# Performance work log

Measured on AMD Instinct MI355X. Metric: run time of the kernel, lower is better.

The kernel has to match this reference:

```python
import jax, jax.numpy as jnp
import numpy as np

B = 2048        # batch
C = 64          # args.embed_size (channel dim; attention runs over this axis)
N = 11          # spatial rows per window
D = 11          # args.hsi_windowSize
SA = N * D      # args.size_SA = 121, Linear in/out size
HID = 128       # args.hid_router
NUM_PATH = 4    # num_out_path


def setup_inputs() -> dict:
    key = jax.random.key(0)
    ks = jax.random.split(key, 12)
    w = lambda k, shape: (jax.random.normal(k, shape, dtype=jnp.float32) * 0.05)
    return {
        "lidar": jax.random.normal(ks[0], (B, C, N, D), dtype=jnp.float32),
        "hsi": jax.random.normal(ks[1], (B, C, N, D), dtype=jnp.float32),
        # Cross_Self_attention linears (shared module, used in both directions)
        "Wq": w(ks[2], (SA, SA)), "bq": jnp.zeros((SA,), jnp.float32),
        "Wk": w(ks[3], (SA, SA)), "bk": jnp.zeros((SA,), jnp.float32),
        "Wv": w(ks[4], (SA, SA)), "bv": jnp.zeros((SA,), jnp.float32),
        # Router MLP: Linear(2C, HID) -> ReLU -> Linear(HID, NUM_PATH) -> softmax
        "Wr1": w(ks[5], (2 * C, HID)), "br1": jnp.zeros((HID,), jnp.float32),
        "Wr2": w(ks[6], (HID, NUM_PATH)), "br2": jnp.zeros((NUM_PATH,), jnp.float32),
        # 1x1 Conv2d(2C -> C): pure channel mixing
        "Wc": w(ks[7], (C, 2 * C)), "bc": jnp.zeros((C,), jnp.float32),
    }


def reference(lidar, hsi, Wq, bq, Wk, bk, Wv, bv, Wr1, br1, Wr2, br2, Wc, bc):
    def cross_sa(x, y):
        # x, y: [B, C, SA]; Linear acts on last dim (size_SA)
        q = x @ Wq.T + bq                                   # [B, C, SA]
        k = x @ Wk.T + bk                                   # [B, C, SA]
        v = y @ Wv.T + bv                                   # [B, C, SA]
        scores = jnp.einsum('bhs,bgs->bhg', q, k)           # [B, C, C] attn over channels
        probs = jax.nn.softmax(scores, axis=-1)
        # custom: attn @ (Q * V) elementwise gate instead of attn @ V
        return jnp.einsum('bhg,bgs->bhs', probs, q * v)     # [B, C, SA]
        # dropout(0.5) is identity in eval mode

    # router on channel-concat of raw inputs
    pooled = jnp.concatenate([lidar, hsi], axis=1).mean(axis=(2, 3))   # [B, 2C]
    path_prob = jax.nn.softmax(jax.nn.relu(pooled @ Wr1 + br1) @ Wr2 + br2, axis=-1)

    l = lidar.reshape(B, C, SA)
    h = hsi.reshape(B, C, SA)
    h_emb = cross_sa(l, h).reshape(B, C, N, D)
    l_emb = cross_sa(h, l).reshape(B, C, N, D)

    cat = jnp.concatenate([l_emb, h_emb], axis=1)                       # [B, 2C, N, D]
    emb = jnp.einsum('oc,bchw->bohw', Wc, cat) + bc[None, :, None, None]
    return (emb, path_prob)
```

## Files before the change

### kernel.cpp

```cpp
#include <hip/hip_runtime.h>
#include <hip/hip_bf16.h>

#define NB 2048
#define SA 121
#define EMB_TOTAL (NB * 64 * SA)

typedef short bf16x8 __attribute__((ext_vector_type(8)));
typedef float f32x4  __attribute__((ext_vector_type(4)));
typedef unsigned int u32x2 __attribute__((ext_vector_type(2)));

__device__ __forceinline__ short f2bf(float f) {
    union { __hip_bfloat16 h; short s; } u;
    u.h = __float2bfloat16(f);
    return u.s;
}
__device__ __forceinline__ unsigned pack2(float a, float b) {
    union { __hip_bfloat16 h[2]; unsigned u; } p;
    p.h[0] = __float2bfloat16(a);
    p.h[1] = __float2bfloat16(b);
    return p.u;
}

#define MFMA(a, b, c) __builtin_amdgcn_mfma_f32_16x16x32_bf16((a), (b), (c), 0, 0, 0)

__global__ void convert_weights(const float* __restrict__ Wq, const float* __restrict__ Wk,
                                const float* __restrict__ Wv, const float* __restrict__ Wc,
                                const float* __restrict__ bq, short* __restrict__ ws) {
    int i = blockIdx.x * 256 + threadIdx.x;
    if (i < 16384) {
        int t = i >> 7, s = i & 127;
        float acc = 0.f;
        if (t < SA && s < SA)
            for (int j = 0; j < SA; ++j) acc += Wq[j * SA + s] * Wk[j * SA + t];
        ws[i] = f2bf(acc);
    } else if (i < 32768) {
        int j = i - 16384; int r = j >> 7, c = j & 127;
        ws[i] = f2bf((r < SA && c < SA) ? Wq[r * SA + c] : 0.f);
    } else if (i < 49152) {
        int j = i - 32768; int r = j >> 7, c = j & 127;
        ws[i] = f2bf((r < SA && c < SA) ? Wv[r * SA + c] : 0.f);
    } else if (i < 57344) {
        ws[i] = f2bf(Wc[i - 49152]);
    } else if (i < 57472) {
        int t = i - 57344;
        float acc = 0.f;
        if (t < SA)
            for (int j = 0; j < SA; ++j) acc += bq[j] * Wk[j * SA + t];
        ((float*)(ws + 57344))[t] = acc;
    }
}

__launch_bounds__(256, 2)
__global__ void fused_kernel(const float* __restrict__ lidar, const float* __restrict__ hsi,
                             const float* __restrict__ bq, const float* __restrict__ bv,
                             const float* __restrict__ Wr1, const float* __restrict__ br1,
                             const float* __restrict__ Wr2, const float* __restrict__ br2,
                             const float* __restrict__ bc,
                             const short* __restrict__ wsb, float* __restrict__ out) {
    __shared__ __align__(16) short sA[64 * 136];
    __shared__ __align__(16) short sB[64 * 136];
    __shared__ __align__(16) short sD[64 * 136];
    __shared__ __align__(16) short sG[128 * 72];
    __shared__ __align__(16) short sE[64 * 72];
    __shared__ float sR[388];

    const int tid  = threadIdx.x;
    const int b    = blockIdx.x;
    const int lane = tid & 63;
    const int wid  = tid >> 6;
    const int l16  = lane & 15;
    const int g16  = lane >> 4;

    const short* WA = wsb;
    const short* WQ = wsb + 16384;
    const short* WV = wsb + 32768;
    const short* WC = wsb + 49152;
    const float* wvp = (const float*)(wsb + 57344);

    bf16x8 wwa[2][4], wqf[2][4], wvf[2][4];
    #pragma unroll
    for (int nn = 0; nn < 2; ++nn) {
        const int rw = ((wid * 2 + nn) * 16 + l16) * 128 + g16 * 8;
        #pragma unroll
        for (int k0 = 0; k0 < 4; ++k0) {
            wwa[nn][k0] = *(const bf16x8*)&WA[rw + k0 * 32];
            wqf[nn][k0] = *(const bf16x8*)&WQ[rw + k0 * 32];
            wvf[nn][k0] = *(const bf16x8*)&WV[rw + k0 * 32];
        }
    }
    bf16x8 wcf[2][2];
    {
        const int rw = (wid * 16 + l16) * 128 + g16 * 8;
        #pragma unroll
        for (int cb = 0; cb < 2; ++cb)
            #pragma unroll
            for (int k0 = 0; k0 < 2; ++k0)
                wcf[cb][k0] = *(const bf16x8*)&WC[rw + cb * 64 + k0 * 32];
    }
    float bqv[2], bvv2[2];
    #pragma unroll
    for (int nn = 0; nn < 2; ++nn) {
        int sc_ = (wid * 2 + nn) * 16 + l16;
        bool ok = sc_ < SA;
        bqv[nn]  = ok ? bq[sc_] : 0.f;
        bvv2[nn] = ok ? bv[sc_] : 0.f;
    }

    {
        const int row = wid * 16 + l16;
        const float* gA = lidar + (size_t)b * 7744 + row * 121;
        const float* gB = hsi   + (size_t)b * 7744 + row * 121;
        float rsA = 0.f, rsB = 0.f, wA = 0.f, wB = 0.f;
        #pragma unroll
        for (int k0 = 0; k0 < 4; ++k0) {
            const int c0 = k0 * 32 + g16 * 8;
            bf16x8 a, h;
            if (c0 == 120) {
                float xa = gA[120], xb = gB[120], wv0 = wvp[120];
                rsA += xa; rsB += xb; wA += xa * wv0; wB += xb * wv0;
                a[0] = f2bf(xa); h[0] = f2bf(xb);
                #pragma unroll
                for (int j = 1; j < 8; ++j) { a[j] = 0; h[j] = 0; }
            } else {
                #pragma unroll
                for (int j = 0; j < 8; ++j) {
                    float xa = gA[c0 + j], xb = gB[c0 + j];
                    float wv0 = wvp[c0 + j];
                    rsA += xa; rsB += xb;
                    wA += xa * wv0; wB += xb * wv0;
                    a[j] = f2bf(xa); h[j] = f2bf(xb);
                }
            }
            *(bf16x8*)&sA[row * 136 + c0] = a;
            *(bf16x8*)&sB[row * 136 + c0] = h;
        }
        rsA += __shfl_xor(rsA, 16, 64); rsA += __shfl_xor(rsA, 32, 64);
        rsB += __shfl_xor(rsB, 16, 64); rsB += __shfl_xor(rsB, 32, 64);
        wA  += __shfl_xor(wA, 16, 64);  wA  += __shfl_xor(wA, 32, 64);
        wB  += __shfl_xor(wB, 16, 64);  wB  += __shfl_xor(wB, 32, 64);
        if (g16 == 0) {
            sR[row] = rsA * (1.f / 121.f);
            sR[64 + row] = rsB * (1.f / 121.f);
            sR[128 + row] = wA;
            sR[192 + row] = wB;
        }
    }
    __syncthreads();

    f32x4 eacc[8];
    #pragma unroll
    for (int n = 0; n < 8; ++n) eacc[n] = (f32x4){0.f, 0.f, 0.f, 0.f};

    #pragma unroll 1
    for (int dir = 0; dir < 2; ++dir) {
        const short* Xqk = dir ? sB : sA;
        const short* Xv  = dir ? sA : sB;
        const int cb = dir ? 0 : 1;

        #pragma unroll
        for (int m = 0; m < 4; ++m) {
            bf16x8 afr[4], vfr[4];
            #pragma unroll
            for (int k0 = 0; k0 < 4; ++k0) {
                afr[k0] = *(const bf16x8*)&Xqk[(m * 16 + l16) * 136 + k0 * 32 + g16 * 8];
                vfr[k0] = *(const bf16x8*)&Xv [(m * 16 + l16) * 136 + k0 * 32 + g16 * 8];
            }
            f32x4 ya[2], qa[2], va[2];
            ya[0] = (f32x4){0,0,0,0}; ya[1] = (f32x4){0,0,0,0};
            qa[0] = (f32x4){0,0,0,0}; qa[1] = (f32x4){0,0,0,0};
            va[0] = (f32x4){0,0,0,0}; va[1] = (f32x4){0,0,0,0};
            #pragma unroll
            for (int k0 = 0; k0 < 4; ++k0) {
                ya[0] = MFMA(afr[k0], wwa[0][k0], ya[0]);
                ya[1] = MFMA(afr[k0], wwa[1][k0], ya[1]);
                qa[0] = MFMA(afr[k0], wqf[0][k0], qa[0]);
                qa[1] = MFMA(afr[k0], wqf[1][k0], qa[1]);
                va[0] = MFMA(vfr[k0], wvf[0][k0], va[0]);
                va[1] = MFMA(vfr[k0], wvf[1][k0], va[1]);
            }
            #pragma unroll
            for (int nn = 0; nn < 2; ++nn) {
                const int sc_ = (wid * 2 + nn) * 16 + l16;
                #pragma unroll
                for (int r = 0; r < 4; ++r)
                    sD[(m * 16 + g16 * 4 + r) * 136 + sc_] = f2bf(ya[nn][r]);
                float g0 = (va[nn][0] + bvv2[nn]) * (qa[nn][0] + bqv[nn]);
                float g1 = (va[nn][1] + bvv2[nn]) * (qa[nn][1] + bqv[nn]);
                float g2 = (va[nn][2] + bvv2[nn]) * (qa[nn][2] + bqv[nn]);
                float g3 = (va[nn][3] + bvv2[nn]) * (qa[nn][3] + bqv[nn]);
                u32x2 pk;
                pk.x = pack2(g0, g1);
                pk.y = pack2(g2, g3);
                *(u32x2*)&sG[sc_ * 72 + m * 16 + g16 * 4] = pk;
            }
        }
        __syncthreads();

        {
            f32x4 sc4[4];
            #pragma unroll
            for (int n = 0; n < 4; ++n) sc4[n] = (f32x4){0,0,0,0};
            #pragma unroll
            for (int k0 = 0; k0 < 4; ++k0) {
                bf16x8 afr = *(const bf16x8*)&sD[(wid * 16 + l16) * 136 + k0 * 32 + g16 * 8];
                #pragma unroll
                for (int n = 0; n < 4; ++n) {
                    bf16x8 bfr = *(const bf16x8*)&Xqk[(n * 16 + l16) * 136 + k0 * 32 + g16 * 8];
                    sc4[n] = MFMA(afr, bfr, sc4[n]);
                }
            }
            float wg[4];
            #pragma unroll
            for (int n = 0; n < 4; ++n) wg[n] = sR[128 + dir * 64 + n * 16 + l16];
            float p[4][4];
            #pragma unroll
            for (int r = 0; r < 4; ++r) {
                float s0 = sc4[0][r] + wg[0], s1 = sc4[1][r] + wg[1];
                float s2 = sc4[2][r] + wg[2], s3 = sc4[3][r] + wg[3];
                float mx = fmaxf(fmaxf(s0, s1), fmaxf(s2, s3));
                #pragma unroll
                for (int off = 1; off < 16; off <<= 1) mx = fmaxf(mx, __shfl_xor(mx, off, 64));
                float e0 = exp2f((s0 - mx) * 1.44269504f);
                float e1 = exp2f((s1 - mx) * 1.44269504f);
                float e2 = exp2f((s2 - mx) * 1.44269504f);
                float e3 = exp2f((s3 - mx) * 1.44269504f);
                float sum = e0 + e1 + e2 + e3;
                #pragma unroll
                for (int off = 1; off < 16; off <<= 1) sum += __shfl_xor(sum, off, 64);
                float inv = 1.f / sum;
                p[0][r] = e0 * inv; p[1][r] = e1 * inv; p[2][r] = e2 * inv; p[3][r] = e3 * inv;
            }
            #pragma unroll
            for (int n = 0; n < 4; ++n) {
                u32x2 pk;
                pk.x = pack2(p[n][0], p[n][1]);
                pk.y = pack2(p[n][2], p[n][3]);
                *(u32x2*)&sE[(n * 16 + l16) * 72 + wid * 16 + g16 * 4] = pk;
            }
        }
        __syncthreads();

        {
            f32x4 macc[4];
            #pragma unroll
            for (int n = 0; n < 4; ++n) macc[n] = (f32x4){0,0,0,0};
            #pragma unroll
            for (int k0 = 0; k0 < 2; ++k0)
                #pragma unroll
                for (int n = 0; n < 4; ++n) {
                    bf16x8 bfr = *(const bf16x8*)&sE[(n * 16 + l16) * 72 + k0 * 32 + g16 * 8];
                    macc[n] = MFMA(wcf[cb][k0], bfr, macc[n]);
                }
            #pragma unroll
            for (int n = 0; n < 4; ++n)
                #pragma unroll
                for (int r = 0; r < 4; ++r)
                    sD[(wid * 16 + g16 * 4 + r) * 72 + n * 16 + l16] = f2bf(macc[n][r]);
        }
        __syncthreads();

        #pragma unroll
        for (int k0 = 0; k0 < 2; ++k0) {
            bf16x8 afr = *(const bf16x8*)&sD[(wid * 16 + l16) * 72 + k0 * 32 + g16 * 8];
            #pragma unroll
            for (int n = 0; n < 8; ++n) {
                bf16x8 bfr = *(const bf16x8*)&sG[(n * 16 + l16) * 72 + k0 * 32 + g16 * 8];
                eacc[n] = MFMA(afr, bfr, eacc[n]);
            }
        }
        __syncthreads();
    }

    float* eo = out + (size_t)b * 7744;
    {
        float bcv[4];
        #pragma unroll
        for (int r = 0; r < 4; ++r) bcv[r] = bc[wid * 16 + g16 * 4 + r];
        #pragma unroll
        for (int n = 0; n < 8; ++n) {
            int s = n * 16 + l16;
            if (s < SA) {
                #pragma unroll
                for (int r = 0; r < 4; ++r) {
                    int o = wid * 16 + g16 * 4 + r;
                    eo[o * 121 + s] = eacc[n][r] + bcv[r];
                }
            }
        }
    }

    if (tid < 128) {
        float a0 = 0.f, a1 = 0.f, a2 = 0.f, a3 = 0.f;
        for (int c = 0; c < 128; c += 4) {
            a0 += sR[c]     * Wr1[(c)     * 128 + tid];
            a1 += sR[c + 1] * Wr1[(c + 1) * 128 + tid];
            a2 += sR[c + 2] * Wr1[(c + 2) * 128 + tid];
            a3 += sR[c + 3] * Wr1[(c + 3) * 128 + tid];
        }
        sR[256 + tid] = fmaxf((a0 + a1) + (a2 + a3) + br1[tid], 0.f);
    }
    __syncthreads();
    if (tid < 4) {
        float a0 = 0.f, a1 = 0.f, a2 = 0.f, a3 = 0.f;
        for (int h = 0; h < 128; h += 4) {
            a0 += sR[256 + h]     * Wr2[(h)     * 4 + tid];
            a1 += sR[256 + h + 1] * Wr2[(h + 1) * 4 + tid];
            a2 += sR[256 + h + 2] * Wr2[(h + 2) * 4 + tid];
            a3 += sR[256 + h + 3] * Wr2[(h + 3) * 4 + tid];
        }
        sR[384 + tid] = (a0 + a1) + (a2 + a3) + br2[tid];
    }
    __syncthreads();
    if (tid < 4) {
        float m = fmaxf(fmaxf(sR[384], sR[385]), fmaxf(sR[386], sR[387]));
        float e = __expf(sR[384 + tid] - m);
        float s = 0.f;
        for (int p = 0; p < 4; ++p) s += __expf(sR[384 + p] - m);
        out[EMB_TOTAL + b * 4 + tid] = e / s;
    }
}

extern "C" void kernel_launch(void* const* d_in, const int* in_sizes, int n_in,
                              void* d_out, int out_size, void* d_ws, size_t ws_size,
                              hipStream_t stream) {
    const float* lidar = (const float*)d_in[0];
    const float* hsi   = (const float*)d_in[1];
    const float* Wq  = (const float*)d_in[2];  const float* bq  = (const float*)d_in[3];
    const float* Wk  = (const float*)d_in[4];
    const float* Wv  = (const float*)d_in[6];  const float* bv  = (const float*)d_in[7];
    const float* Wr1 = (const float*)d_in[8];  const float* br1 = (const float*)d_in[9];
    const float* Wr2 = (const float*)d_in[10]; const float* br2 = (const float*)d_in[11];
    const float* Wc  = (const float*)d_in[12]; const float* bc  = (const float*)d_in[13];
    short* wsb = (short*)d_ws;
    float* out = (float*)d_out;

    hipLaunchKernelGGL(convert_weights, dim3(225), dim3(256), 0, stream, Wq, Wk, Wv, Wc, bq, wsb);
    hipLaunchKernelGGL(fused_kernel, dim3(NB), dim3(256), 0, stream,
                       lidar, hsi, bq, bv, Wr1, br1, Wr2, br2, bc, wsb, out);
}
```

Measured before the change: 114.3 us.

## Merge sD/sG shared buffers by deferring Q*V gate computation to reduce LDS

Drops the separate sG shared buffer. The Q and V projections and their elementwise gate are computed later, after the Wc mixing MFMAs, and written into the reused sD buffer, while the mixed projection now goes to sE. This cuts per-block LDS so more blocks can be resident per CU, at the cost of re-reading the input fragments from LDS in a second pass. The router MLP loops also move to eight independent accumulators for more ILP.

Result: slower. 120.4 us (+5.3%).

```diff
diff --git a/kernel.cpp b/kernel.cpp
--- a/kernel.cpp
+++ b/kernel.cpp
@@ -59,8 +59,7 @@
                              const short* __restrict__ wsb, float* __restrict__ out) {
     __shared__ __align__(16) short sA[64 * 136];
     __shared__ __align__(16) short sB[64 * 136];
-    __shared__ __align__(16) short sD[64 * 136];
-    __shared__ __align__(16) short sG[128 * 72];
+    __shared__ __align__(16) short sD[128 * 72];
     __shared__ __align__(16) short sE[64 * 72];
     __shared__ float sR[388];
 
@@ -158,41 +157,32 @@
         const int cb = dir ? 0 : 1;
 
         #pragma unroll
-        for (int m = 0; m < 4; ++m) {
-            bf16x8 afr[4], vfr[4];
-            #pragma unroll
-            for (int k0 = 0; k0 < 4; ++k0) {
-                afr[k0] = *(const bf16x8*)&Xqk[(m * 16 + l16) * 136 + k0 * 32 + g16 * 8];
-                vfr[k0] = *(const bf16x8*)&Xv [(m * 16 + l16) * 136 + k0 * 32 + g16 * 8];
-            }
-            f32x4 ya[2], qa[2], va[2];
-            ya[0] = (f32x4){0,0,0,0}; ya[1] = (f32x4){0,0,0,0};
-            qa[0] = (f32x4){0,0,0,0}; qa[1] = (f32x4){0,0,0,0};
-            va[0] = (f32x4){0,0,0,0}; va[1] = (f32x4){0,0,0,0};
-            #pragma unroll
-            for (int k0 = 0; k0 < 4; ++k0) {
-                ya[0] = MFMA(afr[k0], wwa[0][k0], ya[0]);
-                ya[1] = MFMA(afr[k0], wwa[1][k0], ya[1]);
-                qa[0] = MFMA(afr[k0], wqf[0][k0], qa[0]);
-                qa[1] = MFMA(afr[k0], wqf[1][k0], qa[1]);
-                va[0] = MFMA(vfr[k0], wvf[0][k0], va[0]);
-                va[1] = MFMA(vfr[k0], wvf[1][k0], va[1]);
-            }
-            #pragma unroll
-            for (int nn = 0; nn < 2; ++nn) {
-                const int sc_ = (wid * 2 + nn) * 16 + l16;
-                #pragma unroll
-                for (int r = 0; r < 4; ++r)
-                    sD[(m * 16 + g16 * 4 + r) * 136 + sc_] = f2bf(ya[nn][r]);
-                float g0 = (va[nn][0] + bvv2[nn]) * (qa[nn][0] + bqv[nn]);
-                float g1 = (va[nn][1] + bvv2[nn]) * (qa[nn][1] + bqv[nn]);
-                float g2 = (va[nn][2] + bvv2[nn]) * (qa[nn][2] + bqv[nn]);
-                float g3 = (va[nn][3] + bvv2[nn]) * (qa[nn][3] + bqv[nn]);
-                u32x2 pk;
-                pk.x = pack2(g0, g1);
-                pk.y = pack2(g2, g3);
-                *(u32x2*)&sG[sc_ * 72 + m * 16 + g16 * 4] = pk;
-            }
+        for (int mp = 0; mp < 2; ++mp) {
+            bf16x8 afr[2][4];
+            #pragma unroll
+            for (int mm = 0; mm < 2; ++mm)
+                #pragma unroll
+                for (int k0 = 0; k0 < 4; ++k0)
+                    afr[mm][k0] = *(const bf16x8*)&Xqk[((mp * 2 + mm) * 16 + l16) * 136 + k0 * 32 + g16 * 8];
+            f32x4 ya[2][2];
+            ya[0][0] = (f32x4){0,0,0,0}; ya[0][1] = (f32x4){0,0,0,0};
+            ya[1][0] = (f32x4){0,0,0,0}; ya[1][1] = (f32x4){0,0,0,0};
+            #pragma unroll
+            for (int k0 = 0; k0 < 4; ++k0)
+                #pragma unroll
+                for (int mm = 0; mm < 2; ++mm) {
+                    ya[mm][0] = MFMA(afr[mm][k0], wwa[0][k0], ya[mm][0]);
+                    ya[mm][1] = MFMA(afr[mm][k0], wwa[1][k0], ya[mm][1]);
+                }
+            #pragma unroll
+            for (int mm = 0; mm < 2; ++mm)
+                #pragma unroll
+                for (int nn = 0; nn < 2; ++nn) {
+                    const int sc_ = (wid * 2 + nn) * 16 + l16;
+                    #pragma unroll
+                    for (int r = 0; r < 4; ++r)
+                        sD[((mp * 2 + mm) * 16 + g16 * 4 + r) * 136 + sc_] = f2bf(ya[mm][nn][r]);
+                }
         }
         __syncthreads();
 
@@ -252,19 +242,50 @@
                     macc[n] = MFMA(wcf[cb][k0], bfr, macc[n]);
                 }
             #pragma unroll
+            for (int m = 0; m < 4; ++m) {
+                bf16x8 afr[4], vfr[4];
+                #pragma unroll
+                for (int k0 = 0; k0 < 4; ++k0) {
+                    afr[k0] = *(const bf16x8*)&Xqk[(m * 16 + l16) * 136 + k0 * 32 + g16 * 8];
+                    vfr[k0] = *(const bf16x8*)&Xv [(m * 16 + l16) * 136 + k0 * 32 + g16 * 8];
+                }
+                f32x4 qa[2], va[2];
+                qa[0] = (f32x4){0,0,0,0}; qa[1] = (f32x4){0,0,0,0};
+                va[0] = (f32x4){0,0,0,0}; va[1] = (f32x4){0,0,0,0};
+                #pragma unroll
+                for (int k0 = 0; k0 < 4; ++k0) {
+                    qa[0] = MFMA(afr[k0], wqf[0][k0], qa[0]);
+                    qa[1] = MFMA(afr[k0], wqf[1][k0], qa[1]);
+                    va[0] = MFMA(vfr[k0], wvf[0][k0], va[0]);
+                    va[1] = MFMA(vfr[k0], wvf[1][k0], va[1]);
+                }
+                #pragma unroll
+                for (int nn = 0; nn < 2; ++nn) {
+                    const int sc_ = (wid * 2 + nn) * 16 + l16;
+                    float g0 = (va[nn][0] + bvv2[nn]) * (qa[nn][0] + bqv[nn]);
+                    float g1 = (va[nn][1] + bvv2[nn]) * (qa[nn][1] + bqv[nn]);
+                    float g2 = (va[nn][2] + bvv2[nn]) * (qa[nn][2] + bqv[nn]);
+                    float g3 = (va[nn][3] + bvv2[nn]) * (qa[nn][3] + bqv[nn]);
+                    u32x2 pk;
+                    pk.x = pack2(g0, g1);
+                    pk.y = pack2(g2, g3);
+                    *(u32x2*)&sD[sc_ * 72 + m * 16 + g16 * 4] = pk;
+                }
+            }
+            __syncthreads();
+            #pragma unroll
             for (int n = 0; n < 4; ++n)
                 #pragma unroll
                 for (int r = 0; r < 4; ++r)
-                    sD[(wid * 16 + g16 * 4 + r) * 72 + n * 16 + l16] = f2bf(macc[n][r]);
-        }
-        __syncthreads();
+                    sE[(wid * 16 + g16 * 4 + r) * 72 + n * 16 + l16] = f2bf(macc[n][r]);
+        }
 
         #pragma unroll
         for (int k0 = 0; k0 < 2; ++k0) {
-            bf16x8 afr = *(const bf16x8*)&sD[(wid * 16 + l16) * 72 + k0 * 32 + g16 * 8];
+            bf16x8 afr = *(const bf16x8*)&sE[(wid * 16 + l16) * 72 + k0 * 32 + g16 * 8];
             #pragma unroll
             for (int n = 0; n < 8; ++n) {
-                bf16x8 bfr = *(const bf16x8*)&sG[(n * 16 + l16) * 72 + k0 * 32 + g16 * 8];
+                bf16x8 bfr = *(const bf16x8*)&sD[(n * 16 + l16) * 72 + k0 * 32 + g16 * 8];
                 eacc[n] = MFMA(afr, bfr, eacc[n]);
             }
         }
@@ -290,25 +311,29 @@
     }
 
     if (tid < 128) {
-        float a0 = 0.f, a1 = 0.f, a2 = 0.f, a3 = 0.f;
-        for (int c = 0; c < 128; c += 4) {
-            a0 += sR[c]     * Wr1[(c)     * 128 + tid];
-            a1 += sR[c + 1] * Wr1[(c + 1) * 128 + tid];
-            a2 += sR[c + 2] * Wr1[(c + 2) * 128 + tid];
-            a3 += sR[c + 3] * Wr1[(c + 3) * 128 + tid];
-        }
-        sR[256 + tid] = fmaxf((a0 + a1) + (a2 + a3) + br1[tid], 0.f);
+        float a[8];
+        #pragma unroll
+        for (int j = 0; j < 8; ++j) a[j] = 0.f;
+        for (int c = 0; c < 128; c += 8) {
+            #pragma unroll
+            for (int j = 0; j < 8; ++j)
+                a[j] += sR[c + j] * Wr1[(c + j) * 128 + tid];
+        }
+        float s01 = a[0] + a[1], s23 = a[2] + a[3], s45 = a[4] + a[5], s67 = a[6] + a[7];
+        sR[256 + tid] = fmaxf((s01 + s23) + (s45 + s67) + br1[tid], 0.f);
     }
     __syncthreads();
     if (tid < 4) {
-        float a0 = 0.f, a1 = 0.f, a2 = 0.f, a3 = 0.f;
-        for (int h = 0; h < 128; h += 4) {
-            a0 += sR[256 + h]     * Wr2[(h)     * 4 + tid];
-            a1 += sR[256 + h + 1] * Wr2[(h + 1) * 4 + tid];
-            a2 += sR[256 + h + 2] * Wr2[(h + 2) * 4 + tid];
-            a3 += sR[256 + h + 3] * Wr2[(h + 3) * 4 + tid];
-        }
-        sR[384 + tid] = (a0 + a1) + (a2 + a3) + br2[tid];
+        float a[8];
+        #pragma unroll
+        for (int j = 0; j < 8; ++j) a[j] = 0.f;
+        for (int h = 0; h < 128; h += 8) {
+            #pragma unroll
+            for (int j = 0; j < 8; ++j)
+                a[j] += sR[256 + h + j] * Wr2[(h + j) * 4 + tid];
+        }
+        float s01 = a[0] + a[1], s23 = a[2] + a[3], s45 = a[4] + a[5], s67 = a[6] + a[7];
+        sR[384 + tid] = (s01 + s23) + (s45 + s67) + br2[tid];
     }
     __syncthreads();
     if (tid < 4) {
```
